# Performance work log

Measured on AMD Instinct MI355X. Metric: run time of the kernel, lower is better.

The kernel has to match this reference:

```python
import jax, jax.numpy as jnp
import numpy as np

N = 50000
E = 800000
D = 128


def setup_inputs() -> dict:
    key = jax.random.key(0)
    ks = jax.random.split(key, 6)
    x = jax.random.normal(ks[0], (N, D), dtype=jnp.float32)
    edge_index = jax.random.randint(ks[1], (2, E), 0, N, dtype=jnp.int32)
    scale = 1.0 / np.sqrt(D)
    Ws = jax.random.uniform(ks[2], (D, D), jnp.float32, -scale, scale)
    bs = jax.random.uniform(ks[3], (D,), jnp.float32, -scale, scale)
    Wn = jax.random.uniform(ks[4], (D, D), jnp.float32, -scale, scale)
    bn = jax.random.uniform(ks[5], (D,), jnp.float32, -scale, scale)
    return {"x": x, "edge_index": edge_index, "Ws": Ws, "bs": bs, "Wn": Wn, "bn": bn}


def reference(x, edge_index, Ws, bs, Wn, bn):
    # x: [N, D]; edge_index: [2, E] with rows (src, dst)
    src = edge_index[0]
    dst = edge_index[1]
    n = x.shape[0]
    # scatter-sum of gathered source features onto destinations
    agg = jax.ops.segment_sum(x[src], dst, num_segments=n)  # [N, D]
    deg = jax.ops.segment_sum(jnp.ones(dst.shape, x.dtype), dst, num_segments=n)  # [N]
    neigh = agg / jnp.clip(deg, 1.0)[:, None]  # mean aggregation, clamp deg>=1
    # torch Linear: y = x @ W.T + b
    return jax.nn.relu(x @ Ws.T + bs + neigh @ Wn.T + bn)
```

## Files before the change

### kernel.cpp

```cpp
#include <hip/hip_runtime.h>

#define D 128
#define CAP 64
#define NXCD 8
#define CHUNK 2048

typedef short bf16x8 __attribute__((ext_vector_type(8)));
typedef float f32x4 __attribute__((ext_vector_type(4)));

__device__ __forceinline__ unsigned f2bf(float f) {
    unsigned u = __builtin_bit_cast(unsigned, f);
    return (u + 0x7FFFu + ((u >> 16) & 1u)) >> 16;
}
__device__ __forceinline__ float bflo(unsigned u) {
    return __builtin_bit_cast(float, u << 16);
}
__device__ __forceinline__ float bfhi(unsigned u) {
    return __builtin_bit_cast(float, u & 0xFFFF0000u);
}

__global__ __launch_bounds__(256)
void sage_prep(const float* __restrict__ x,
               const float* __restrict__ Ws,
               const float* __restrict__ Wn,
               const int* __restrict__ ei,
               unsigned short* __restrict__ xb,
               unsigned short* __restrict__ Wsb,
               unsigned short* __restrict__ Wnb,
               unsigned short* __restrict__ srcs,
               int* __restrict__ cnt,
               int nD4, int DD4, int bucketBlocks, int E, int nodesPerXcd)
{
    const int tid = threadIdx.x;
    if ((int)blockIdx.x < bucketBlocks) {
        const int xcd = blockIdx.x & (NXCD - 1);
        const int lo = xcd * nodesPerXcd;
        const int hi = lo + nodesPerXcd;
        const int e0 = (blockIdx.x >> 3) * CHUNK + tid * 8;
        if (e0 < E) {
            const int4* sp = reinterpret_cast<const int4*>(ei + e0);
            const int4* dp = reinterpret_cast<const int4*>(ei + E + e0);
            int4 sA = sp[0], sB = sp[1];
            int4 dA = dp[0], dB = dp[1];
            int ss[8] = {sA.x, sA.y, sA.z, sA.w, sB.x, sB.y, sB.z, sB.w};
            int dd[8] = {dA.x, dA.y, dA.z, dA.w, dB.x, dB.y, dB.z, dB.w};
            #pragma unroll
            for (int q = 0; q < 8; ++q) {
                int dst = dd[q];
                if (dst >= lo && dst < hi) {
                    int pos = atomicAdd(&cnt[dst], 1);
                    if (pos < CAP) srcs[dst * CAP + pos] = (unsigned short)ss[q];
                }
            }
        }
    } else {
        int i4 = (blockIdx.x - bucketBlocks) * 256 + tid;
        const float* src; unsigned short* dst; int off;
        if (i4 < nD4)                { src = x;  dst = xb;  off = i4; }
        else if (i4 < nD4 + DD4)     { src = Ws; dst = Wsb; off = i4 - nD4; }
        else if (i4 < nD4 + 2 * DD4) { src = Wn; dst = Wnb; off = i4 - nD4 - DD4; }
        else return;
        float4 v = reinterpret_cast<const float4*>(src)[off];
        ushort4 o;
        o.x = (unsigned short)f2bf(v.x);
        o.y = (unsigned short)f2bf(v.y);
        o.z = (unsigned short)f2bf(v.z);
        o.w = (unsigned short)f2bf(v.w);
        reinterpret_cast<ushort4*>(dst)[off] = o;
    }
}

__global__ __launch_bounds__(512)
void sage_fused(const unsigned short* __restrict__ xb,
                const unsigned short* __restrict__ srcs,
                const int* __restrict__ cnt,
                const unsigned short* __restrict__ Wsb,
                const unsigned short* __restrict__ Wnb,
                const float* __restrict__ bs,
                const float* __restrict__ bn,
                float* __restrict__ out, int n)
{
    __shared__ unsigned nlds[16 * 64];
    const int lane = threadIdx.x & 63;
    const int w = threadIdx.x >> 6;
    const int g = lane >> 4;
    const int gl = lane & 15;
    const int r0 = blockIdx.x * 16;

    #pragma unroll
    for (int i = 0; i < 2; ++i) {
        const int nl = w * 2 + i;
        const int node = r0 + nl;
        int c = cnt[node];
        c = c > CAP ? CAP : c;
        float s[8] = {0.f, 0.f, 0.f, 0.f, 0.f, 0.f, 0.f, 0.f};
        if (c > 0) {
            unsigned idtab = reinterpret_cast<const unsigned*>(
                srcs + (size_t)node * CAP)[lane & 31];
            const char* xbase = (const char*)xb + (gl << 4);
            for (int kb = 0; kb < c; kb += 16) {
                uint4 v[4];
                int jv[4];
                #pragma unroll
                for (int q = 0; q < 4; ++q) {
                    int j = kb + q * 4 + g;
                    jv[q] = j;
                    int jj = j < c ? j : c - 1;
                    unsigned uv = __builtin_amdgcn_ds_bpermute((jj >> 1) << 2,
                                                               (int)idtab);
                    unsigned id = (uv >> ((jj & 1) << 4)) & 0xFFFFu;
                    v[q] = *reinterpret_cast<const uint4*>(xbase + ((size_t)id << 8));
                }
                #pragma unroll
                for (int q = 0; q < 4; ++q) {
                    unsigned m = jv[q] < c ? 0xFFFFFFFFu : 0u;
                    unsigned a0 = v[q].x & m, a1 = v[q].y & m,
                             a2 = v[q].z & m, a3 = v[q].w & m;
                    s[0] += bflo(a0); s[1] += bfhi(a0);
                    s[2] += bflo(a1); s[3] += bfhi(a1);
                    s[4] += bflo(a2); s[5] += bfhi(a2);
                    s[6] += bflo(a3); s[7] += bfhi(a3);
                }
            }
            #pragma unroll
            for (int q = 0; q < 8; ++q) {
                s[q] += __shfl_xor(s[q], 16);
                s[q] += __shfl_xor(s[q], 32);
            }
        }
        if (g == 0) {
            float inv = 1.f / fmaxf((float)c, 1.f);
            uint4 o;
            o.x = f2bf(s[0] * inv) | (f2bf(s[1] * inv) << 16);
            o.y = f2bf(s[2] * inv) | (f2bf(s[3] * inv) << 16);
            o.z = f2bf(s[4] * inv) | (f2bf(s[5] * inv) << 16);
            o.w = f2bf(s[6] * inv) | (f2bf(s[7] * inv) << 16);
            *reinterpret_cast<uint4*>(
                (char*)nlds + nl * 256 + ((gl << 4) ^ ((nl & 7) << 4))) = o;
        }
    }
    __syncthreads();

    const int jl = lane & 15;
    const int arow = r0 + jl;
    const int kq = (lane >> 4) * 8;

    const unsigned short* xrow = xb + (size_t)arow * D + kq;
    const char* lbase = (const char*)nlds + jl * 256;
    const unsigned sw = (unsigned)((jl & 7) << 4);
    bf16x8 axf[4], anf[4];
    #pragma unroll
    for (int ks = 0; ks < 4; ++ks) {
        axf[ks] = *reinterpret_cast<const bf16x8*>(xrow + ks * 32);
        anf[ks] = *reinterpret_cast<const bf16x8*>(
            lbase + (((unsigned)((kq << 1) + (ks << 6))) ^ sw));
    }

    const int j = w * 16 + jl;
    const unsigned short* wsrow = Wsb + (size_t)j * D + kq;
    const unsigned short* wnrow = Wnb + (size_t)j * D + kq;
    f32x4 acc = {0.f, 0.f, 0.f, 0.f};
    #pragma unroll
    for (int ks = 0; ks < 4; ++ks) {
        bf16x8 bsf = *reinterpret_cast<const bf16x8*>(wsrow + ks * 32);
        bf16x8 bnf = *reinterpret_cast<const bf16x8*>(wnrow + ks * 32);
        acc = __builtin_amdgcn_mfma_f32_16x16x32_bf16(axf[ks], bsf, acc, 0, 0, 0);
        acc = __builtin_amdgcn_mfma_f32_16x16x32_bf16(anf[ks], bnf, acc, 0, 0, 0);
    }
    const float bias = bs[j] + bn[j];
    const int outrow0 = r0 + (lane >> 4) * 4;
    #pragma unroll
    for (int r = 0; r < 4; ++r) {
        float vv = acc[r] + bias;
        out[(size_t)(outrow0 + r) * D + j] = vv > 0.f ? vv : 0.f;
    }
}

extern "C" void kernel_launch(void* const* d_in, const int* in_sizes, int n_in,
                              void* d_out, int out_size, void* d_ws, size_t ws_size,
                              hipStream_t stream)
{
    const float* x  = (const float*)d_in[0];
    const int*   ei = (const int*)d_in[1];
    const float* Ws = (const float*)d_in[2];
    const float* bs = (const float*)d_in[3];
    const float* Wn = (const float*)d_in[4];
    const float* bn = (const float*)d_in[5];
    float* out = (float*)d_out;

    const int n = in_sizes[0] / D;
    const int E = in_sizes[1] / 2;

    unsigned short* xb   = (unsigned short*)d_ws;
    unsigned short* srcs = xb + (size_t)n * D;
    int*            cnt  = (int*)(srcs + (size_t)n * CAP);
    unsigned short* Wsb  = (unsigned short*)(cnt + n);
    unsigned short* Wnb  = Wsb + D * D;

    hipMemsetAsync(cnt, 0, (size_t)n * sizeof(int), stream);

    const int nD4 = n * D / 4;
    const int DD4 = D * D / 4;
    const int chunks       = (E + CHUNK - 1) / CHUNK;
    const int bucketBlocks = chunks * NXCD;
    const int convBlocks   = (nD4 + 2 * DD4 + 255) / 256;
    const int nodesPerXcd  = (n + NXCD - 1) / NXCD;

    sage_prep<<<bucketBlocks + convBlocks, 256, 0, stream>>>(
        x, Ws, Wn, ei, xb, Wsb, Wnb, srcs, cnt, nD4, DD4, bucketBlocks, E,
        nodesPerXcd);

    {
        int tiles = n / 16;
        sage_fused<<<tiles, 512, 0, stream>>>(xb, srcs, cnt, Wsb, Wnb,
                                              bs, bn, out, n);
    }
}
```

Measured before the change: 181.0 us.

## Split fused gather+GEMM into separate column-split gather and MFMA kernels

Replaces the single fused kernel with two. The first gathers and mean-aggregates neighbours, splitting the 128 feature columns across 4 blocks per 16-node tile so more blocks and smaller 8-byte loads are in flight; it writes fp32 neighbour means into the output buffer. The second kernel reads those rows back, converts them to bf16 and runs the MFMA linear layers, one wave per 16-row tile covering all 128 output columns. This aims to decouple the latency-bound gather from the GEMM and raise gather parallelism, at the cost of an extra launch plus a full fp32 N×D write and re-read through the output buffer.

```diff
diff --git a/kernel.cpp b/kernel.cpp
--- a/kernel.cpp
+++ b/kernel.cpp
@@ -70,109 +70,115 @@
     }
 }
 
-__global__ __launch_bounds__(512)
-void sage_fused(const unsigned short* __restrict__ xb,
-                const unsigned short* __restrict__ srcs,
-                const int* __restrict__ cnt,
-                const unsigned short* __restrict__ Wsb,
-                const unsigned short* __restrict__ Wnb,
-                const float* __restrict__ bs,
-                const float* __restrict__ bn,
-                float* __restrict__ out, int n)
-{
-    __shared__ unsigned nlds[16 * 64];
+__global__ __launch_bounds__(256)
+void sage_gather(const unsigned short* __restrict__ xb,
+                 const unsigned short* __restrict__ srcs,
+                 const int* __restrict__ cnt,
+                 float* __restrict__ neighF, int n)
+{
     const int lane = threadIdx.x & 63;
     const int w = threadIdx.x >> 6;
-    const int g = lane >> 4;
-    const int gl = lane & 15;
-    const int r0 = blockIdx.x * 16;
+    const int tile = blockIdx.x >> 2;
+    const int cg = blockIdx.x & 3;
+    const int g = lane >> 3;
+    const int gl = lane & 7;
+
+    const char* xbase = (const char*)xb + cg * 64 + gl * 8;
 
     #pragma unroll
-    for (int i = 0; i < 2; ++i) {
-        const int nl = w * 2 + i;
-        const int node = r0 + nl;
+    for (int i = 0; i < 4; ++i) {
+        const int node = tile * 16 + w * 4 + i;
         int c = cnt[node];
         c = c > CAP ? CAP : c;
-        float s[8] = {0.f, 0.f, 0.f, 0.f, 0.f, 0.f, 0.f, 0.f};
+        float s0 = 0.f, s1 = 0.f, s2 = 0.f, s3 = 0.f;
         if (c > 0) {
             unsigned idtab = reinterpret_cast<const unsigned*>(
                 srcs + (size_t)node * CAP)[lane & 31];
-            const char* xbase = (const char*)xb + (gl << 4);
             for (int kb = 0; kb < c; kb += 16) {
-                uint4 v[4];
-                int jv[4];
                 #pragma unroll
-                for (int q = 0; q < 4; ++q) {
-                    int j = kb + q * 4 + g;
-                    jv[q] = j;
+                for (int q = 0; q < 2; ++q) {
+                    int j = kb + q * 8 + g;
                     int jj = j < c ? j : c - 1;
                     unsigned uv = __builtin_amdgcn_ds_bpermute((jj >> 1) << 2,
                                                                (int)idtab);
                     unsigned id = (uv >> ((jj & 1) << 4)) & 0xFFFFu;
-                    v[q] = *reinterpret_cast<const uint4*>(xbase + ((size_t)id << 8));
-                }
-                #pragma unroll
-                for (int q = 0; q < 4; ++q) {
-                    unsigned m = jv[q] < c ? 0xFFFFFFFFu : 0u;
-                    unsigned a0 = v[q].x & m, a1 = v[q].y & m,
-                             a2 = v[q].z & m, a3 = v[q].w & m;
-                    s[0] += bflo(a0); s[1] += bfhi(a0);
-                    s[2] += bflo(a1); s[3] += bfhi(a1);
-                    s[4] += bflo(a2); s[5] += bfhi(a2);
-                    s[6] += bflo(a3); s[7] += bfhi(a3);
+                    uint2 v = *reinterpret_cast<const uint2*>(
+                        xbase + ((size_t)id << 8));
+                    unsigned m = j < c ? 0xFFFFFFFFu : 0u;
+                    unsigned a0 = v.x & m, a1 = v.y & m;
+                    s0 += bflo(a0); s1 += bfhi(a0);
+                    s2 += bflo(a1); s3 += bfhi(a1);
                 }
             }
-            #pragma unroll
-            for (int q = 0; q < 8; ++q) {
-                s[q] += __shfl_xor(s[q], 16);
-                s[q] += __shfl_xor(s[q], 32);
-            }
+            s0 += __shfl_xor(s0, 8);  s1 += __shfl_xor(s1, 8);
+            s2 += __shfl_xor(s2, 8);  s3 += __shfl_xor(s3, 8);
+            s0 += __shfl_xor(s0, 16); s1 += __shfl_xor(s1, 16);
+            s2 += __shfl_xor(s2, 16); s3 += __shfl_xor(s3, 16);
+            s0 += __shfl_xor(s0, 32); s1 += __shfl_xor(s1, 32);
+            s2 += __shfl_xor(s2, 32); s3 += __shfl_xor(s3, 32);
         }
         if (g == 0) {
             float inv = 1.f / fmaxf((float)c, 1.f);
-            uint4 o;
-            o.x = f2bf(s[0] * inv) | (f2bf(s[1] * inv) << 16);
-            o.y = f2bf(s[2] * inv) | (f2bf(s[3] * inv) << 16);
-            o.z = f2bf(s[4] * inv) | (f2bf(s[5] * inv) << 16);
-            o.w = f2bf(s[6] * inv) | (f2bf(s[7] * inv) << 16);
-            *reinterpret_cast<uint4*>(
-                (char*)nlds + nl * 256 + ((gl << 4) ^ ((nl & 7) << 4))) = o;
-        }
-    }
-    __syncthreads();
-
-    const int jl = lane & 15;
-    const int arow = r0 + jl;
-    const int kq = (lane >> 4) * 8;
+            float4 o = {s0 * inv, s1 * inv, s2 * inv, s3 * inv};
+            *reinterpret_cast<float4*>(
+                neighF + (size_t)node * D + cg * 32 + gl * 4) = o;
+        }
+    }
+}
+
+__global__ __launch_bounds__(256)
+void sage_mfma(const unsigned short* __restrict__ xb,
+               const float* nF,
+               const unsigned short* __restrict__ Wsb,
+               const unsigned short* __restrict__ Wnb,
+               const float* __restrict__ bs,
+               const float* __restrict__ bn,
+               float* out, int ntiles)
+{
+    int wave = (blockIdx.x * blockDim.x + threadIdx.x) >> 6;
+    if (wave >= ntiles) return;
+    int lane = threadIdx.x & 63;
+    int r0 = wave * 16;
+    int arow = r0 + (lane & 15);
+    int kq = (lane >> 4) * 8;
 
     const unsigned short* xrow = xb + (size_t)arow * D + kq;
-    const char* lbase = (const char*)nlds + jl * 256;
-    const unsigned sw = (unsigned)((jl & 7) << 4);
+    const float* nrow = nF + (size_t)arow * D + kq;
     bf16x8 axf[4], anf[4];
-    #pragma unroll
+#pragma unroll
     for (int ks = 0; ks < 4; ++ks) {
         axf[ks] = *reinterpret_cast<const bf16x8*>(xrow + ks * 32);
-        anf[ks] = *reinterpret_cast<const bf16x8*>(
-            lbase + (((unsigned)((kq << 1) + (ks << 6))) ^ sw));
-    }
-
-    const int j = w * 16 + jl;
-    const unsigned short* wsrow = Wsb + (size_t)j * D + kq;
-    const unsigned short* wnrow = Wnb + (size_t)j * D + kq;
-    f32x4 acc = {0.f, 0.f, 0.f, 0.f};
-    #pragma unroll
-    for (int ks = 0; ks < 4; ++ks) {
-        bf16x8 bsf = *reinterpret_cast<const bf16x8*>(wsrow + ks * 32);
-        bf16x8 bnf = *reinterpret_cast<const bf16x8*>(wnrow + ks * 32);
-        acc = __builtin_amdgcn_mfma_f32_16x16x32_bf16(axf[ks], bsf, acc, 0, 0, 0);
-        acc = __builtin_amdgcn_mfma_f32_16x16x32_bf16(anf[ks], bnf, acc, 0, 0, 0);
-    }
-    const float bias = bs[j] + bn[j];
+        float4 f0 = *reinterpret_cast<const float4*>(nrow + ks * 32);
+        float4 f1 = *reinterpret_cast<const float4*>(nrow + ks * 32 + 4);
+        bf16x8 t;
+        t[0] = (short)f2bf(f0.x); t[1] = (short)f2bf(f0.y);
+        t[2] = (short)f2bf(f0.z); t[3] = (short)f2bf(f0.w);
+        t[4] = (short)f2bf(f1.x); t[5] = (short)f2bf(f1.y);
+        t[6] = (short)f2bf(f1.z); t[7] = (short)f2bf(f1.w);
+        anf[ks] = t;
+    }
+
+    const int jl = lane & 15;
     const int outrow0 = r0 + (lane >> 4) * 4;
-    #pragma unroll
-    for (int r = 0; r < 4; ++r) {
-        float vv = acc[r] + bias;
-        out[(size_t)(outrow0 + r) * D + j] = vv > 0.f ? vv : 0.f;
+#pragma unroll
+    for (int c = 0; c < 8; ++c) {
+        int j = c * 16 + jl;
+        const unsigned short* wsrow = Wsb + (size_t)j * D + kq;
+        const unsigned short* wnrow = Wnb + (size_t)j * D + kq;
+        f32x4 acc = {0.f, 0.f, 0.f, 0.f};
+#pragma unroll
+        for (int ks = 0; ks < 4; ++ks) {
+            bf16x8 bsf = *reinterpret_cast<const bf16x8*>(wsrow + ks * 32);
+            bf16x8 bnf = *reinterpret_cast<const bf16x8*>(wnrow + ks * 32);
+            acc = __builtin_amdgcn_mfma_f32_16x16x32_bf16(axf[ks], bsf, acc, 0, 0, 0);
+            acc = __builtin_amdgcn_mfma_f32_16x16x32_bf16(anf[ks], bnf, acc, 0, 0, 0);
+        }
+        float bias = bs[j] + bn[j];
+#pragma unroll
+        for (int r = 0; r < 4; ++r) {
+            float v = acc[r] + bias;
+            out[(size_t)(outrow0 + r) * D + j] = v > 0.f ? v : 0.f;
+        }
     }
 }
 
@@ -212,7 +218,13 @@
 
     {
         int tiles = n / 16;
-        sage_fused<<<tiles, 512, 0, stream>>>(xb, srcs, cnt, Wsb, Wnb,
-                                              bs, bn, out, n);
-    }
-}
+        sage_gather<<<tiles * 4, 256, 0, stream>>>(xb, srcs, cnt, out, n);
+    }
+
+    {
+        int ntiles = n / 16;
+        int blocks = (ntiles * 64 + 255) / 256;
+        sage_mfma<<<blocks, 256, 0, stream>>>(xb, out, Wsb, Wnb, bs, bn,
+                                              out, ntiles);
+    }
+}
```

After: 211.5 us. +16.8%, slower.
